# Performance work log

Hardware: AMD Instinct MI355X
Metric: run time of the kernel (lower is better)

## Reference

```python
import jax, jax.numpy as jnp
import numpy as np

B, N, E = 2, 50000, 800000
IN, HID, OUT = 128, 64, 1
EPS = 1e-5


def setup_inputs() -> dict:
    key = jax.random.key(0)
    ks = jax.random.split(key, 13)
    x = jax.random.normal(ks[0], (B, N, IN), jnp.float32)
    edge_index = jax.random.randint(ks[1], (2, E), 0, N, dtype=jnp.int64)
    edge_weight = 0.1 * jax.random.normal(ks[2], (E,), jnp.float32)  # nn.Parameter, pre-exp
    W1 = jax.random.normal(ks[3], (IN, HID), jnp.float32) / np.sqrt(IN)
    b1 = jnp.zeros((HID,), jnp.float32)
    W2 = jax.random.normal(ks[4], (HID, HID), jnp.float32) / np.sqrt(HID)
    b2 = jnp.zeros((HID,), jnp.float32)
    g1 = jnp.ones((HID,), jnp.float32)
    be1 = jnp.zeros((HID,), jnp.float32)
    g2 = jnp.ones((HID,), jnp.float32)
    be2 = jnp.zeros((HID,), jnp.float32)
    Wc = jax.random.normal(ks[5], (HID, OUT), jnp.float32) / np.sqrt(HID)
    bc = jnp.zeros((OUT,), jnp.float32)
    return {"x": x, "edge_weight": edge_weight, "W1": W1, "b1": b1,
            "W2": W2, "b2": b2, "g1": g1, "be1": be1, "g2": g2, "be2": be2,
            "Wc": Wc, "bc": bc, "edge_index": edge_index}


def reference(x, edge_weight, W1, b1, W2, b2, g1, be1, g2, be2, Wc, bc, edge_index):
    n = x.shape[1]
    row, col = edge_index[0], edge_index[1]
    ew = jnp.exp(edge_weight)
    # GCN normalization with self-loops (fill_value=1), as in PyG gcn_norm
    loop = jnp.arange(n)
    rows = jnp.concatenate([row, loop])
    cols = jnp.concatenate([col, loop])
    w = jnp.concatenate([ew, jnp.ones((n,), ew.dtype)])
    deg = jax.ops.segment_sum(w, cols, num_segments=n)
    dinv = 1.0 / jnp.sqrt(deg)  # deg >= 1 due to self-loops
    norm = dinv[rows] * w * dinv[cols]  # [E+N]

    def conv(h, W, b):
        h = h @ W                                  # [B, N, H]
        msg = h[:, rows, :] * norm[None, :, None]  # gather + weight  [B, E+N, H]
        agg = jnp.zeros_like(h).at[:, cols, :].add(msg)  # scatter-add
        return agg + b

    def bn(h, g, be):  # BatchNorm1d over flattened (B*N, H), training-mode stats
        h2 = h.reshape(-1, h.shape[-1])
        m = h2.mean(axis=0)
        v = h2.var(axis=0)
        return (((h2 - m) / jnp.sqrt(v + EPS)) * g + be).reshape(h.shape)

    h = jax.nn.relu(conv(x, W1, b1))
    h = bn(h, g1, be1)  # dropout is identity in eval
    h = jax.nn.relu(conv(h, W2, b2))
    h = bn(h, g2, be2)
    out = (h @ Wc + bc)[..., 0]  # squeeze(-1) -> [B, N]
    return out
```

## Files before the change

### kernel.cpp

```cpp
#include <hip/hip_runtime.h>
#include <hip/hip_fp16.h>
#include <cstdint>
#include <cstddef>


#define CAP  64
#define OCAP 65536
#define BN_EPS 1e-5f

static __device__ __forceinline__ unsigned h2u(__half2 h) {
  union { __half2 h; unsigned u; } c; c.h = h; return c.u;
}
static __device__ __forceinline__ __half2 u2h(unsigned u) {
  union { unsigned u; __half2 h; } c; c.u = u; return c.h;
}

__global__ void k_deg(const float* __restrict__ ew, const int* __restrict__ ei,
                      float* __restrict__ deg, int E) {
  int e = blockIdx.x * blockDim.x + threadIdx.x;
  if (e < E) atomicAdd(&deg[ei[(size_t)E + e]], expf(ew[e]));
}

__global__ void k_dinv(float* __restrict__ deg, int N) {
  int i = blockIdx.x * blockDim.x + threadIdx.x;
  if (i < N) deg[i] = rsqrtf(deg[i] + 1.0f);
}

__global__ void k_fill(const float* __restrict__ ew, const int* __restrict__ ei,
                       const float* __restrict__ dinv, int* __restrict__ cnt,
                       int2* __restrict__ pairs,
                       int* __restrict__ ofl_cnt, int* __restrict__ ofl_list, int E) {
  int e = blockIdx.x * blockDim.x + threadIdx.x;
  if (e >= E) return;
  int r = ei[e];
  int c = ei[(size_t)E + e];
  float nrm = dinv[r] * expf(ew[e]) * dinv[c];
  int pos = atomicAdd(&cnt[c], 1);
  if (pos < CAP) {
    pairs[(size_t)c * CAP + pos] = make_int2(r, __float_as_int(nrm));
  } else {
    int o = atomicAdd(ofl_cnt, 1);
    if (o < OCAP) ofl_list[o] = e;
  }
}

template<int CIN, bool TR, bool PERM>
__global__ void k_gemm(const void* __restrict__ in_, const float* __restrict__ W,
                       __half* __restrict__ out, int nrows, int N,
                       const float* __restrict__ bias, const float* __restrict__ scsh) {
  constexpr int RT = 64;
  constexpr int XS = CIN + 4;
  constexpr int KV = CIN / 4;
  __shared__ float ws[CIN * 64];
  __shared__ float xs[RT * XS];

  int tid = threadIdx.x;
  int row0 = blockIdx.x * RT;

  for (int s = tid; s < CIN * 16; s += 256)
    ((float4*)ws)[s] = ((const float4*)W)[s];

  for (int s = tid; s < RT * KV; s += 256) {
    int r = s / KV, k4 = s - r * KV;
    int gr = row0 + r;
    float4 v = make_float4(0.f, 0.f, 0.f, 0.f);
    if (gr < nrows) {
      if (TR) {
        const __half* in = (const __half*)in_;
        uint2 u = *(const uint2*)(in + (size_t)gr * CIN + k4 * 4);
        float2 fa = __half22float2(u2h(u.x));
        float2 fb = __half22float2(u2h(u.y));
        v = make_float4(fa.x, fa.y, fb.x, fb.y);
      } else {
        const float* in = (const float*)in_;
        v = *(const float4*)(in + (size_t)gr * CIN + k4 * 4);
      }
    }
    if (TR) {
      float4 bb = *(const float4*)(bias + k4 * 4);
      float4 sc = *(const float4*)(scsh + k4 * 4);
      float4 sh = *(const float4*)(scsh + 64 + k4 * 4);
      v.x = fmaxf(v.x + bb.x, 0.f) * sc.x + sh.x;
      v.y = fmaxf(v.y + bb.y, 0.f) * sc.y + sh.y;
      v.z = fmaxf(v.z + bb.z, 0.f) * sc.z + sh.z;
      v.w = fmaxf(v.w + bb.w, 0.f) * sc.w + sh.w;
    }
    *(float4*)&xs[r * XS + k4 * 4] = v;
  }
  __syncthreads();

  int rg = tid >> 4;
  int cg = tid & 15;
  int c0 = cg * 4;
  int r0 = rg * 4;

  float acc[4][4];
#pragma unroll
  for (int i = 0; i < 4; ++i)
#pragma unroll
    for (int j = 0; j < 4; ++j) acc[i][j] = 0.0f;

#pragma unroll 2
  for (int k = 0; k < CIN; k += 4) {
    float4 wv0 = *(const float4*)&ws[(k + 0) * 64 + c0];
    float4 wv1 = *(const float4*)&ws[(k + 1) * 64 + c0];
    float4 wv2 = *(const float4*)&ws[(k + 2) * 64 + c0];
    float4 wv3 = *(const float4*)&ws[(k + 3) * 64 + c0];
#pragma unroll
    for (int i = 0; i < 4; ++i) {
      float4 xv = *(const float4*)&xs[(r0 + i) * XS + k];
      acc[i][0] = fmaf(xv.x, wv0.x, acc[i][0]);
      acc[i][1] = fmaf(xv.x, wv0.y, acc[i][1]);
      acc[i][2] = fmaf(xv.x, wv0.z, acc[i][2]);
      acc[i][3] = fmaf(xv.x, wv0.w, acc[i][3]);
      acc[i][0] = fmaf(xv.y, wv1.x, acc[i][0]);
      acc[i][1] = fmaf(xv.y, wv1.y, acc[i][1]);
      acc[i][2] = fmaf(xv.y, wv1.z, acc[i][2]);
      acc[i][3] = fmaf(xv.y, wv1.w, acc[i][3]);
      acc[i][0] = fmaf(xv.z, wv2.x, acc[i][0]);
      acc[i][1] = fmaf(xv.z, wv2.y, acc[i][1]);
      acc[i][2] = fmaf(xv.z, wv2.z, acc[i][2]);
      acc[i][3] = fmaf(xv.z, wv2.w, acc[i][3]);
      acc[i][0] = fmaf(xv.w, wv3.x, acc[i][0]);
      acc[i][1] = fmaf(xv.w, wv3.y, acc[i][1]);
      acc[i][2] = fmaf(xv.w, wv3.z, acc[i][2]);
      acc[i][3] = fmaf(xv.w, wv3.w, acc[i][3]);
    }
  }

#pragma unroll
  for (int i = 0; i < 4; ++i) {
    int gr = row0 + r0 + i;
    if (gr < nrows) {
      int orow = PERM ? ((gr < N) ? gr * 2 : (gr - N) * 2 + 1) : gr;
      __half2 h01 = __floats2half2_rn(acc[i][0], acc[i][1]);
      __half2 h23 = __floats2half2_rn(acc[i][2], acc[i][3]);
      *(uint2*)(out + (size_t)orow * 64 + c0) = make_uint2(h2u(h01), h2u(h23));
    }
  }
}

__global__ void k_agg(const __half* __restrict__ h, const int2* __restrict__ pairs,
                      const int* __restrict__ cnt, const float* __restrict__ dinv,
                      __half* __restrict__ raw, int N) {
  int node = blockIdx.x * 4 + (threadIdx.x >> 6);
  if (node >= N) return;
  int lane = threadIdx.x & 63;
  const __half2* hv = (const __half2*)h;
  float d = dinv[node];
  d = d * d;
  float2 self = __half22float2(hv[(size_t)node * 64 + lane]);
  float2 acc = make_float2(self.x * d, self.y * d);
  int n = cnt[node];
  n = n > CAP ? CAP : n;
  const int2* pp = pairs + (size_t)node * CAP;
  int k = 0;
  for (; k + 8 <= n; k += 8) {
    int2 p[8];
#pragma unroll
    for (int q = 0; q < 8; ++q) p[q] = pp[k + q];
    __half2 v[8];
#pragma unroll
    for (int q = 0; q < 8; ++q) v[q] = hv[(size_t)p[q].x * 64 + lane];
#pragma unroll
    for (int q = 0; q < 8; ++q) {
      float w = __int_as_float(p[q].y);
      float2 f = __half22float2(v[q]);
      acc.x = fmaf(w, f.x, acc.x);
      acc.y = fmaf(w, f.y, acc.y);
    }
  }
  for (; k < n; ++k) {
    int2 p = pp[k];
    float2 f = __half22float2(hv[(size_t)p.x * 64 + lane]);
    float w = __int_as_float(p.y);
    acc.x = fmaf(w, f.x, acc.x);
    acc.y = fmaf(w, f.y, acc.y);
  }
  ((__half2*)raw)[(size_t)node * 64 + lane] = __floats2half2_rn(acc.x, acc.y);
}

__global__ void k_ofl(const float* __restrict__ ew, const int* __restrict__ ei,
                      const float* __restrict__ dinv, const int* __restrict__ ofl_cnt,
                      const int* __restrict__ ofl_list,
                      const __half* __restrict__ h, __half* __restrict__ raw,
                      int N, int E) {
  int tot = *ofl_cnt;
  if (tot > OCAP) tot = OCAP;
  for (int i = blockIdx.x * blockDim.x + threadIdx.x; i < tot;
       i += gridDim.x * blockDim.x) {
    int e = ofl_list[i];
    int r = ei[e];
    int c = ei[(size_t)E + e];
    float nrm = dinv[r] * expf(ew[e]) * dinv[c];
    const __half2* hr = (const __half2*)(h + (size_t)r * 128);
    unsigned* dst = (unsigned*)(raw + (size_t)c * 128);
    for (int j = 0; j < 64; ++j) {
      float2 hv2 = __half22float2(hr[j]);
      unsigned old = dst[j], assumed;
      do {
        assumed = old;
        float2 cur = __half22float2(u2h(assumed));
        __half2 nv = __floats2half2_rn(cur.x + nrm * hv2.x, cur.y + nrm * hv2.y);
        old = atomicCAS(&dst[j], assumed, h2u(nv));
      } while (old != assumed);
    }
  }
}

__global__ void k_stats(const __half* __restrict__ raw, const float* __restrict__ bias,
                        float* __restrict__ stats, int rows) {
  __shared__ float S[256], Q[256];
  int tid = threadIdx.x;
  int c = tid & 63, rg = tid >> 6;
  float s = 0.0f, q = 0.0f;
  for (int r = blockIdx.x * 4 + rg; r < rows; r += gridDim.x * 4) {
    float y = fmaxf(__half2float(raw[(size_t)r * 64 + c]) + bias[c], 0.0f);
    s += y;
    q += y * y;
  }
  S[tid] = s; Q[tid] = q;
  __syncthreads();
  if (tid < 64) {
    float ts = S[tid] + S[tid + 64] + S[tid + 128] + S[tid + 192];
    float tq = Q[tid] + Q[tid + 64] + Q[tid + 128] + Q[tid + 192];
    atomicAdd(&stats[tid], ts);
    atomicAdd(&stats[64 + tid], tq);
  }
}

__global__ void k_scale(const float* __restrict__ stats, const float* __restrict__ g,
                        const float* __restrict__ be, float* __restrict__ scsh,
                        float invCnt) {
  int c = threadIdx.x;
  if (c >= 64) return;
  float m = stats[c] * invCnt;
  float v = stats[64 + c] * invCnt - m * m;
  v = v < 0.0f ? 0.0f : v;
  float inv = rsqrtf(v + BN_EPS);
  float sc = g[c] * inv;
  scsh[c] = sc;
  scsh[64 + c] = be[c] - m * sc;
}

__global__ void k_out(const __half* __restrict__ raw, const float* __restrict__ bias,
                      const float* __restrict__ scsh, const float* __restrict__ Wc,
                      const float* __restrict__ bc, float* __restrict__ out,
                      int rows, int N) {
  int row = blockIdx.x * 4 + (threadIdx.x >> 6);
  int c = threadIdx.x & 63;
  if (row >= rows) return;
  float v = fmaxf(__half2float(raw[(size_t)row * 64 + c]) + bias[c], 0.0f)
              * scsh[c] + scsh[64 + c];
  float p = v * Wc[c];
#pragma unroll
  for (int off = 32; off > 0; off >>= 1) p += __shfl_xor(p, off, 64);
  if (c == 0) {
    int node = row >> 1, b = row & 1;
    out[(size_t)b * N + node] = p + bc[0];
  }
}

extern "C" void kernel_launch(void* const* d_in, const int* in_sizes, int n_in,
                              void* d_out, int out_size, void* d_ws, size_t ws_size,
                              hipStream_t stream) {
  const float* x   = (const float*)d_in[0];
  const float* ew  = (const float*)d_in[1];
  const float* W1  = (const float*)d_in[2];
  const float* b1  = (const float*)d_in[3];
  const float* W2  = (const float*)d_in[4];
  const float* b2  = (const float*)d_in[5];
  const float* g1  = (const float*)d_in[6];
  const float* be1 = (const float*)d_in[7];
  const float* g2  = (const float*)d_in[8];
  const float* be2 = (const float*)d_in[9];
  const float* Wc  = (const float*)d_in[10];
  const float* bc  = (const float*)d_in[11];
  const int*   ei  = (const int*)d_in[12];

  const int E  = in_sizes[1];
  const int BN = in_sizes[0] / 128;
  const int N  = BN / 2;

  char* w = (char*)d_ws;
  size_t off = 0;
  float* dinv   = (float*)(w + off); off += (size_t)N * 4;
  int*   cnt    = (int*)  (w + off); off += (size_t)N * 4;
  float* stats1 = (float*)(w + off); off += 512;
  float* stats2 = (float*)(w + off); off += 512;
  int*   oflc   = (int*)  (w + off); off += 16;
  size_t zbytes = off;
  float* scsh1  = (float*)(w + off); off += 512;
  float* scsh2  = (float*)(w + off); off += 512;
  int*   ofll   = (int*)  (w + off); off += (size_t)OCAP * 4;
  off = (off + 255) & ~(size_t)255;
  int2*   pairs = (int2*)  (w + off); off += (size_t)N * CAP * 8;
  __half* bufA  = (__half*)(w + off); off += (size_t)BN * 64 * 2;
  __half* bufB  = (__half*)(w + off); off += (size_t)BN * 64 * 2;

  float* out = (float*)d_out;

  hipMemsetAsync(w, 0, zbytes, stream);

  dim3 blk(256);
  int gE  = (E + 255) / 256;
  int gN  = (N + 255) / 256;
  int gG  = (BN + 63) / 64;
  int gR  = (BN + 3) / 4;
  int gA  = (N + 3) / 4;

  k_deg<<<gE, blk, 0, stream>>>(ew, ei, dinv, E);
  k_dinv<<<gN, blk, 0, stream>>>(dinv, N);
  k_fill<<<gE, blk, 0, stream>>>(ew, ei, dinv, cnt, pairs, oflc, ofll, E);

  k_gemm<128, false, true><<<gG, blk, 0, stream>>>(x, W1, bufA, BN, N, nullptr, nullptr);
  k_agg<<<gA, blk, 0, stream>>>(bufA, pairs, cnt, dinv, bufB, N);
  k_ofl<<<16, blk, 0, stream>>>(ew, ei, dinv, oflc, ofll, bufA, bufB, N, E);
  k_stats<<<400, blk, 0, stream>>>(bufB, b1, stats1, BN);
  k_scale<<<1, 64, 0, stream>>>(stats1, g1, be1, scsh1, 1.0f / (float)BN);

  k_gemm<64, true, false><<<gG, blk, 0, stream>>>(bufB, W2, bufA, BN, N, b1, scsh1);
  k_agg<<<gA, blk, 0, stream>>>(bufA, pairs, cnt, dinv, bufB, N);
  k_ofl<<<16, blk, 0, stream>>>(ew, ei, dinv, oflc, ofll, bufA, bufB, N, E);
  k_stats<<<400, blk, 0, stream>>>(bufB, b2, stats2, BN);
  k_scale<<<1, 64, 0, stream>>>(stats2, g2, be2, scsh2, 1.0f / (float)BN);

  k_out<<<gR, blk, 0, stream>>>(bufB, b2, scsh2, Wc, bc, out, BN, N);
}
```

Before: 394.3 us.

## Compute degrees from bucketed pairs and apply dinv inside aggregation

The atomic degree pass over all edges is removed. The fill kernel now stores the raw exp weight and handles four edges per thread, and a new per-node wave reduction over the bucketed pairs computes degrees, with a separate kernel for overflow edges. Aggregation multiplies by dinv[row] per neighbour and by dinv[col] once at the end, which adds a gather per edge in each of the two layers. The GEMM now stages the input dimension in 64-wide chunks, which cuts shared memory use for the 128-input layer and may allow higher occupancy.

```diff
diff --git a/kernel.cpp b/kernel.cpp
--- a/kernel.cpp
+++ b/kernel.cpp
@@ -15,33 +15,68 @@
   union { unsigned u; __half2 h; } c; c.u = u; return c.h;
 }
 
-__global__ void k_deg(const float* __restrict__ ew, const int* __restrict__ ei,
-                      float* __restrict__ deg, int E) {
-  int e = blockIdx.x * blockDim.x + threadIdx.x;
-  if (e < E) atomicAdd(&deg[ei[(size_t)E + e]], expf(ew[e]));
-}
-
-__global__ void k_dinv(float* __restrict__ deg, int N) {
+__global__ void k_fill(const float* __restrict__ ew, const int* __restrict__ ei,
+                       int* __restrict__ cnt, int2* __restrict__ pairs,
+                       int* __restrict__ ofl_cnt, int* __restrict__ ofl_list, int E) {
+  int i0 = blockIdx.x * 1024 + threadIdx.x;
+  int r[4], c[4];
+  float w[4];
+  bool ok[4];
+#pragma unroll
+  for (int j = 0; j < 4; ++j) {
+    int e = i0 + j * 256;
+    ok[j] = e < E;
+    if (ok[j]) {
+      r[j] = ei[e];
+      c[j] = ei[(size_t)E + e];
+      w[j] = expf(ew[e]);
+    }
+  }
+  int pos[4];
+#pragma unroll
+  for (int j = 0; j < 4; ++j)
+    if (ok[j]) pos[j] = atomicAdd(&cnt[c[j]], 1);
+#pragma unroll
+  for (int j = 0; j < 4; ++j) {
+    if (!ok[j]) continue;
+    if (pos[j] < CAP) {
+      pairs[(size_t)c[j] * CAP + pos[j]] = make_int2(r[j], __float_as_int(w[j]));
+    } else {
+      int o = atomicAdd(ofl_cnt, 1);
+      if (o < OCAP) ofl_list[o] = i0 + j * 256;
+    }
+  }
+}
+
+__global__ void k_degb(const int2* __restrict__ pairs, const int* __restrict__ cnt,
+                       float* __restrict__ deg, int N) {
+  int node = blockIdx.x * 4 + (threadIdx.x >> 6);
+  if (node >= N) return;
+  int lane = threadIdx.x & 63;
+  int n = cnt[node];
+  n = n > CAP ? CAP : n;
+  float v = 0.0f;
+  if (lane < n) v = __int_as_float(pairs[(size_t)node * CAP + lane].y);
+#pragma unroll
+  for (int off = 32; off > 0; off >>= 1) v += __shfl_xor(v, off, 64);
+  if (lane == 0) deg[node] = v + 1.0f;
+}
+
+__global__ void k_dego(const float* __restrict__ ew, const int* __restrict__ ei,
+                       const int* __restrict__ ofl_cnt, const int* __restrict__ ofl_list,
+                       float* __restrict__ deg, int E) {
+  int tot = *ofl_cnt;
+  if (tot > OCAP) tot = OCAP;
+  for (int i = blockIdx.x * blockDim.x + threadIdx.x; i < tot;
+       i += gridDim.x * blockDim.x) {
+    int e = ofl_list[i];
+    atomicAdd(&deg[ei[(size_t)E + e]], expf(ew[e]));
+  }
+}
+
+__global__ void k_dinvf(float* __restrict__ deg, int N) {
   int i = blockIdx.x * blockDim.x + threadIdx.x;
-  if (i < N) deg[i] = rsqrtf(deg[i] + 1.0f);
-}
-
-__global__ void k_fill(const float* __restrict__ ew, const int* __restrict__ ei,
-                       const float* __restrict__ dinv, int* __restrict__ cnt,
-                       int2* __restrict__ pairs,
-                       int* __restrict__ ofl_cnt, int* __restrict__ ofl_list, int E) {
-  int e = blockIdx.x * blockDim.x + threadIdx.x;
-  if (e >= E) return;
-  int r = ei[e];
-  int c = ei[(size_t)E + e];
-  float nrm = dinv[r] * expf(ew[e]) * dinv[c];
-  int pos = atomicAdd(&cnt[c], 1);
-  if (pos < CAP) {
-    pairs[(size_t)c * CAP + pos] = make_int2(r, __float_as_int(nrm));
-  } else {
-    int o = atomicAdd(ofl_cnt, 1);
-    if (o < OCAP) ofl_list[o] = e;
-  }
+  if (i < N) deg[i] = rsqrtf(deg[i]);
 }
 
 template<int CIN, bool TR, bool PERM>
@@ -49,46 +84,14 @@
                        __half* __restrict__ out, int nrows, int N,
                        const float* __restrict__ bias, const float* __restrict__ scsh) {
   constexpr int RT = 64;
-  constexpr int XS = CIN + 4;
-  constexpr int KV = CIN / 4;
-  __shared__ float ws[CIN * 64];
-  __shared__ float xs[RT * XS];
+  constexpr int KC = 64;
+  constexpr int NCH = CIN / KC;
+  constexpr int S = KC + 4;
+  __shared__ float ws[KC * 64];
+  __shared__ float xs[RT * S];
 
   int tid = threadIdx.x;
   int row0 = blockIdx.x * RT;
-
-  for (int s = tid; s < CIN * 16; s += 256)
-    ((float4*)ws)[s] = ((const float4*)W)[s];
-
-  for (int s = tid; s < RT * KV; s += 256) {
-    int r = s / KV, k4 = s - r * KV;
-    int gr = row0 + r;
-    float4 v = make_float4(0.f, 0.f, 0.f, 0.f);
-    if (gr < nrows) {
-      if (TR) {
-        const __half* in = (const __half*)in_;
-        uint2 u = *(const uint2*)(in + (size_t)gr * CIN + k4 * 4);
-        float2 fa = __half22float2(u2h(u.x));
-        float2 fb = __half22float2(u2h(u.y));
-        v = make_float4(fa.x, fa.y, fb.x, fb.y);
-      } else {
-        const float* in = (const float*)in_;
-        v = *(const float4*)(in + (size_t)gr * CIN + k4 * 4);
-      }
-    }
-    if (TR) {
-      float4 bb = *(const float4*)(bias + k4 * 4);
-      float4 sc = *(const float4*)(scsh + k4 * 4);
-      float4 sh = *(const float4*)(scsh + 64 + k4 * 4);
-      v.x = fmaxf(v.x + bb.x, 0.f) * sc.x + sh.x;
-      v.y = fmaxf(v.y + bb.y, 0.f) * sc.y + sh.y;
-      v.z = fmaxf(v.z + bb.z, 0.f) * sc.z + sh.z;
-      v.w = fmaxf(v.w + bb.w, 0.f) * sc.w + sh.w;
-    }
-    *(float4*)&xs[r * XS + k4 * 4] = v;
-  }
-  __syncthreads();
-
   int rg = tid >> 4;
   int cg = tid & 15;
   int c0 = cg * 4;
@@ -100,31 +103,67 @@
 #pragma unroll
     for (int j = 0; j < 4; ++j) acc[i][j] = 0.0f;
 
+  for (int ch = 0; ch < NCH; ++ch) {
+    if (ch) __syncthreads();
+    const float4* Wp = (const float4*)(W + (size_t)ch * KC * 64);
+    for (int s = tid; s < KC * 16; s += 256)
+      ((float4*)ws)[s] = Wp[s];
+    for (int s = tid; s < RT * 16; s += 256) {
+      int r = s >> 4, k4 = s & 15;
+      int gr = row0 + r;
+      int kg = ch * KC + k4 * 4;
+      float4 v = make_float4(0.f, 0.f, 0.f, 0.f);
+      if (gr < nrows) {
+        if (TR) {
+          const __half* in = (const __half*)in_;
+          uint2 u = *(const uint2*)(in + (size_t)gr * CIN + kg);
+          float2 fa = __half22float2(u2h(u.x));
+          float2 fb = __half22float2(u2h(u.y));
+          v = make_float4(fa.x, fa.y, fb.x, fb.y);
+        } else {
+          const float* in = (const float*)in_;
+          v = *(const float4*)(in + (size_t)gr * CIN + kg);
+        }
+      }
+      if (TR) {
+        float4 bb = *(const float4*)(bias + kg);
+        float4 sc = *(const float4*)(scsh + kg);
+        float4 sh = *(const float4*)(scsh + 64 + kg);
+        v.x = fmaxf(v.x + bb.x, 0.f) * sc.x + sh.x;
+        v.y = fmaxf(v.y + bb.y, 0.f) * sc.y + sh.y;
+        v.z = fmaxf(v.z + bb.z, 0.f) * sc.z + sh.z;
+        v.w = fmaxf(v.w + bb.w, 0.f) * sc.w + sh.w;
+      }
+      *(float4*)&xs[r * S + k4 * 4] = v;
+    }
+    __syncthreads();
+
 #pragma unroll 2
-  for (int k = 0; k < CIN; k += 4) {
-    float4 wv0 = *(const float4*)&ws[(k + 0) * 64 + c0];
-    float4 wv1 = *(const float4*)&ws[(k + 1) * 64 + c0];
-    float4 wv2 = *(const float4*)&ws[(k + 2) * 64 + c0];
-    float4 wv3 = *(const float4*)&ws[(k + 3) * 64 + c0];
-#pragma unroll
-    for (int i = 0; i < 4; ++i) {
-      float4 xv = *(const float4*)&xs[(r0 + i) * XS + k];
-      acc[i][0] = fmaf(xv.x, wv0.x, acc[i][0]);
-      acc[i][1] = fmaf(xv.x, wv0.y, acc[i][1]);
-      acc[i][2] = fmaf(xv.x, wv0.z, acc[i][2]);
-      acc[i][3] = fmaf(xv.x, wv0.w, acc[i][3]);
-      acc[i][0] = fmaf(xv.y, wv1.x, acc[i][0]);
-      acc[i][1] = fmaf(xv.y, wv1.y, acc[i][1]);
-      acc[i][2] = fmaf(xv.y, wv1.z, acc[i][2]);
-      acc[i][3] = fmaf(xv.y, wv1.w, acc[i][3]);
-      acc[i][0] = fmaf(xv.z, wv2.x, acc[i][0]);
-      acc[i][1] = fmaf(xv.z, wv2.y, acc[i][1]);
-      acc[i][2] = fmaf(xv.z, wv2.z, acc[i][2]);
-      acc[i][3] = fmaf(xv.z, wv2.w, acc[i][3]);
-      acc[i][0] = fmaf(xv.w, wv3.x, acc[i][0]);
-      acc[i][1] = fmaf(xv.w, wv3.y, acc[i][1]);
-      acc[i][2] = fmaf(xv.w, wv3.z, acc[i][2]);
-      acc[i][3] = fmaf(xv.w, wv3.w, acc[i][3]);
+    for (int kk = 0; kk < KC; kk += 4) {
+      float4 wv0 = *(const float4*)&ws[(kk + 0) * 64 + c0];
+      float4 wv1 = *(const float4*)&ws[(kk + 1) * 64 + c0];
+      float4 wv2 = *(const float4*)&ws[(kk + 2) * 64 + c0];
+      float4 wv3 = *(const float4*)&ws[(kk + 3) * 64 + c0];
+#pragma unroll
+      for (int i = 0; i < 4; ++i) {
+        float4 xv = *(const float4*)&xs[(r0 + i) * S + kk];
+        acc[i][0] = fmaf(xv.x, wv0.x, acc[i][0]);
+        acc[i][1] = fmaf(xv.x, wv0.y, acc[i][1]);
+        acc[i][2] = fmaf(xv.x, wv0.z, acc[i][2]);
+        acc[i][3] = fmaf(xv.x, wv0.w, acc[i][3]);
+        acc[i][0] = fmaf(xv.y, wv1.x, acc[i][0]);
+        acc[i][1] = fmaf(xv.y, wv1.y, acc[i][1]);
+        acc[i][2] = fmaf(xv.y, wv1.z, acc[i][2]);
+        acc[i][3] = fmaf(xv.y, wv1.w, acc[i][3]);
+        acc[i][0] = fmaf(xv.z, wv2.x, acc[i][0]);
+        acc[i][1] = fmaf(xv.z, wv2.y, acc[i][1]);
+        acc[i][2] = fmaf(xv.z, wv2.z, acc[i][2]);
+        acc[i][3] = fmaf(xv.z, wv2.w, acc[i][3]);
+        acc[i][0] = fmaf(xv.w, wv3.x, acc[i][0]);
+        acc[i][1] = fmaf(xv.w, wv3.y, acc[i][1]);
+        acc[i][2] = fmaf(xv.w, wv3.z, acc[i][2]);
+        acc[i][3] = fmaf(xv.w, wv3.w, acc[i][3]);
+      }
     }
   }
 
@@ -147,10 +186,9 @@
   if (node >= N) return;
   int lane = threadIdx.x & 63;
   const __half2* hv = (const __half2*)h;
-  float d = dinv[node];
-  d = d * d;
+  float dc = dinv[node];
   float2 self = __half22float2(hv[(size_t)node * 64 + lane]);
-  float2 acc = make_float2(self.x * d, self.y * d);
+  float2 acc = make_float2(self.x * dc, self.y * dc);
   int n = cnt[node];
   n = n > CAP ? CAP : n;
   const int2* pp = pairs + (size_t)node * CAP;
@@ -159,12 +197,15 @@
     int2 p[8];
 #pragma unroll
     for (int q = 0; q < 8; ++q) p[q] = pp[k + q];
+    float dr[8];
+#pragma unroll
+    for (int q = 0; q < 8; ++q) dr[q] = dinv[p[q].x];
     __half2 v[8];
 #pragma unroll
     for (int q = 0; q < 8; ++q) v[q] = hv[(size_t)p[q].x * 64 + lane];
 #pragma unroll
     for (int q = 0; q < 8; ++q) {
-      float w = __int_as_float(p[q].y);
+      float w = __int_as_float(p[q].y) * dr[q];
       float2 f = __half22float2(v[q]);
       acc.x = fmaf(w, f.x, acc.x);
       acc.y = fmaf(w, f.y, acc.y);
@@ -172,12 +213,13 @@
   }
   for (; k < n; ++k) {
     int2 p = pp[k];
+    float w = __int_as_float(p.y) * dinv[p.x];
     float2 f = __half22float2(hv[(size_t)p.x * 64 + lane]);
-    float w = __int_as_float(p.y);
     acc.x = fmaf(w, f.x, acc.x);
     acc.y = fmaf(w, f.y, acc.y);
   }
-  ((__half2*)raw)[(size_t)node * 64 + lane] = __floats2half2_rn(acc.x, acc.y);
+  ((__half2*)raw)[(size_t)node * 64 + lane] =
+      __floats2half2_rn(acc.x * dc, acc.y * dc);
 }
 
 __global__ void k_ofl(const float* __restrict__ ew, const int* __restrict__ ei,
@@ -303,15 +345,16 @@
   hipMemsetAsync(w, 0, zbytes, stream);
 
   dim3 blk(256);
-  int gE  = (E + 255) / 256;
+  int gE4 = (E + 1023) / 1024;
   int gN  = (N + 255) / 256;
   int gG  = (BN + 63) / 64;
   int gR  = (BN + 3) / 4;
   int gA  = (N + 3) / 4;
 
-  k_deg<<<gE, blk, 0, stream>>>(ew, ei, dinv, E);
-  k_dinv<<<gN, blk, 0, stream>>>(dinv, N);
-  k_fill<<<gE, blk, 0, stream>>>(ew, ei, dinv, cnt, pairs, oflc, ofll, E);
+  k_fill<<<gE4, blk, 0, stream>>>(ew, ei, cnt, pairs, oflc, ofll, E);
+  k_degb<<<gA, blk, 0, stream>>>(pairs, cnt, dinv, N);
+  k_dego<<<16, blk, 0, stream>>>(ew, ei, oflc, ofll, dinv, E);
+  k_dinvf<<<gN, blk, 0, stream>>>(dinv, N);
 
   k_gemm<128, false, true><<<gG, blk, 0, stream>>>(x, W1, bufA, BN, N, nullptr, nullptr);
   k_agg<<<gA, blk, 0, stream>>>(bufA, pairs, cnt, dinv, bufB, N);
```

Result: faster. 362.4 us (-8.1%).
